# Performance work log

Measured on AMD Instinct MI355X. Metric: run time of the kernel, lower is better.

The kernel has to match this reference:

```python
import jax, jax.numpy as jnp
import numpy as np

B, D, H, R, OUT = 16384, 1024, 4, 1024, 10
LN_EPS = 1e-5


def setup_inputs() -> dict:
    key = jax.random.key(0)
    ks = jax.random.split(key, 20)
    s_in = 1.0 / np.sqrt(D)
    s_hid = 1.0 / np.sqrt(H * R)
    inp = {
        'x': jax.random.normal(ks[0], (B, D), dtype=jnp.float32),
        # block 1
        'wr1': jax.random.normal(ks[1], (H, R, D), dtype=jnp.float32) * s_in,
        'br1': jnp.zeros((H, R), dtype=jnp.float32),
        'wl1': jax.random.normal(ks[2], (H, R, D), dtype=jnp.float32) * s_in,
        'bl1': jnp.zeros((H, R), dtype=jnp.float32),
        'we1': jax.random.normal(ks[3], (D, H * R), dtype=jnp.float32) * s_hid,
        'be1': jnp.zeros((D,), dtype=jnp.float32),
        'g1': jnp.ones((D,), dtype=jnp.float32),
        'b1': jnp.zeros((D,), dtype=jnp.float32),
        # block 2
        'wr2': jax.random.normal(ks[4], (H, R, D), dtype=jnp.float32) * s_in,
        'br2': jnp.zeros((H, R), dtype=jnp.float32),
        'wl2': jax.random.normal(ks[5], (H, R, D), dtype=jnp.float32) * s_in,
        'bl2': jnp.zeros((H, R), dtype=jnp.float32),
        'we2': jax.random.normal(ks[6], (D, H * R), dtype=jnp.float32) * s_hid,
        'be2': jnp.zeros((D,), dtype=jnp.float32),
        'g2': jnp.ones((D,), dtype=jnp.float32),
        'b2': jnp.zeros((D,), dtype=jnp.float32),
        # final linear
        'wf': jax.random.normal(ks[7], (OUT, D), dtype=jnp.float32) * s_in,
        'bf': jnp.zeros((OUT,), dtype=jnp.float32),
    }
    return inp


def _bilinear_block(x, wr, br, wl, bl, we, be):
    # per-basis right/left projections batched into one einsum each: [B,D] x [H,R,D] -> [B,H,R]
    right = jnp.einsum('bd,hrd->bhr', x, wr) + br
    left = jnp.einsum('bd,hrd->bhr', x, wl) + bl
    # elementwise bilinear interaction, concat bases along last dim -> [B, H*R]
    inter = (right * left).reshape(x.shape[0], -1)
    return inter @ we.T + be  # [B, D_out]


def _layernorm(x, g, b):
    mu = jnp.mean(x, axis=-1, keepdims=True)
    var = jnp.mean(jnp.square(x - mu), axis=-1, keepdims=True)
    return (x - mu) * jax.lax.rsqrt(var + LN_EPS) * g + b


def reference(x, wr1, br1, wl1, bl1, we1, be1, g1, b1,
              wr2, br2, wl2, bl2, we2, be2, g2, b2, wf, bf):
    # block 1: bilinear + residual + layernorm
    h = _layernorm(x + _bilinear_block(x, wr1, br1, wl1, bl1, we1, be1), g1, b1)
    # block 2
    h = _layernorm(h + _bilinear_block(h, wr2, br2, wl2, bl2, we2, be2), g2, b2)
    # final linear head
    return h @ wf.T + bf
```

## Files before the change

### kernel.cpp

```cpp
#include <hip/hip_runtime.h>
#include <hip/hip_fp16.h>

#define DEV static __device__ __forceinline__

typedef _Float16 f16;
typedef _Float16 f16x8 __attribute__((ext_vector_type(8)));
typedef _Float16 f16x4 __attribute__((ext_vector_type(4)));
typedef float f32x4 __attribute__((ext_vector_type(4)));

constexpr int BATCH = 16384;
constexpr int D = 1024;
constexpr int HR = 4096;
constexpr int NOUT = 10;

__global__ void k_f32_to_f16(const float* __restrict__ src, f16* __restrict__ dst, int n4) {
    int i = blockIdx.x * blockDim.x + threadIdx.x;
    int stride = gridDim.x * blockDim.x;
    for (; i < n4; i += stride) {
        float4 v = reinterpret_cast<const float4*>(src)[i];
        f16x4 h;
        h[0] = (f16)v.x; h[1] = (f16)v.y; h[2] = (f16)v.z; h[3] = (f16)v.w;
        reinterpret_cast<f16x4*>(dst)[i] = h;
    }
}

DEV void stage16(void* lds, const void* g) {
    __builtin_amdgcn_global_load_lds(
        (const __attribute__((address_space(1))) void*)g,
        (__attribute__((address_space(3))) void*)lds,
        16, 0, 0);
}

DEV const char* src_ptr(const void* base, int tid, int row0, int rowBytes) {
    const int r = tid >> 2;
    const int cb = ((tid & 3) << 4) ^ (((r >> 1) & 3) << 4);
    return (const char*)base + (size_t)(row0 + r) * rowBytes + cb;
}

DEV int xcd_swz(int bid, int nwg) {
    const int cpx = nwg >> 3;
    return (bid & 7) * cpx + (bid >> 3);
}

__global__ __launch_bounds__(512, 2) void k_gemm_dual(
    const f16* __restrict__ Xh, const f16* __restrict__ Wr, const f16* __restrict__ Wl,
    const float* __restrict__ br, const float* __restrict__ bl,
    f16* __restrict__ inter, int MT)
{
    extern __shared__ __align__(16) char smem[];
    constexpr int K = 1024, NT = K / 32;
    constexpr int BUF = 32 * 1024;

    const int swz = xcd_swz(blockIdx.x, gridDim.x);
    const int mt = swz % MT, nt = swz / MT;
    const int m0 = mt * 256, n0 = nt * 128;
    const int tid = threadIdx.x;
    const int wid = tid >> 6, lane = tid & 63;
    const int wm = wid >> 2, wn = wid & 3;
    const int fr = lane & 15, fq = lane >> 4;
    const int colb = (fq << 4) ^ (((fr >> 1) & 3) << 4);

    const char* sA0 = src_ptr(Xh, tid, m0,       2048);
    const char* sA1 = src_ptr(Xh, tid, m0 + 128, 2048);
    const char* sR  = src_ptr(Wr, tid, n0,       2048);
    const char* sL  = src_ptr(Wl, tid, n0,       2048);
    const int dA0 = tid * 16, dA1 = 8192 + tid * 16;
    const int dR = 16384 + tid * 16, dL = 24576 + tid * 16;

    f32x4 accR[8][2] = {};
    f32x4 accL[8][2] = {};

    for (int t = 0; t < 2; ++t) {
        char* b = smem + t * BUF;
        const long ko = (long)t * 64;
        stage16(b + dA0, sA0 + ko);  stage16(b + dA1, sA1 + ko);
        stage16(b + dR,  sR  + ko);  stage16(b + dL,  sL  + ko);
    }
    asm volatile("s_waitcnt vmcnt(4)" ::: "memory");
    __builtin_amdgcn_s_barrier();

    int cur = 0;
    long koff = 128;
    for (int t = 0; t < NT; ++t) {
        char* base = smem + cur * BUF;
        const int stg = cur ? cur - 1 : 2;
        char* nb = smem + stg * BUF;
        const bool pf = (t + 2) < NT;

        f16x8 a[4], bR[2], bL[2];
#pragma unroll
        for (int m = 0; m < 4; ++m)
            a[m] = *(const f16x8*)(base + (wm * 128 + m * 16 + fr) * 64 + colb);
#pragma unroll
        for (int n = 0; n < 2; ++n) {
            bR[n] = *(const f16x8*)(base + 16384 + (wn * 32 + n * 16 + fr) * 64 + colb);
            bL[n] = *(const f16x8*)(base + 24576 + (wn * 32 + n * 16 + fr) * 64 + colb);
        }
        if (pf) { stage16(nb + dA0, sA0 + koff);  stage16(nb + dA1, sA1 + koff); }
        __builtin_amdgcn_s_barrier();
        __builtin_amdgcn_s_setprio(1);
#pragma unroll
        for (int m = 0; m < 4; ++m)
#pragma unroll
            for (int n = 0; n < 2; ++n) {
                accR[m][n] = __builtin_amdgcn_mfma_f32_16x16x32_f16(a[m], bR[n], accR[m][n], 0, 0, 0);
                accL[m][n] = __builtin_amdgcn_mfma_f32_16x16x32_f16(a[m], bL[n], accL[m][n], 0, 0, 0);
            }
        __builtin_amdgcn_s_setprio(0);
        __builtin_amdgcn_s_barrier();

        f16x8 a2[4];
#pragma unroll
        for (int m = 0; m < 4; ++m)
            a2[m] = *(const f16x8*)(base + (wm * 128 + (4 + m) * 16 + fr) * 64 + colb);
        if (pf) { stage16(nb + dR, sR + koff);  stage16(nb + dL, sL + koff); }
        __builtin_amdgcn_s_barrier();
        __builtin_amdgcn_s_setprio(1);
#pragma unroll
        for (int m = 0; m < 4; ++m)
#pragma unroll
            for (int n = 0; n < 2; ++n) {
                accR[4 + m][n] = __builtin_amdgcn_mfma_f32_16x16x32_f16(a2[m], bR[n], accR[4 + m][n], 0, 0, 0);
                accL[4 + m][n] = __builtin_amdgcn_mfma_f32_16x16x32_f16(a2[m], bL[n], accL[4 + m][n], 0, 0, 0);
            }
        __builtin_amdgcn_s_setprio(0);
        if (t < NT - 1) {
            if (pf) asm volatile("s_waitcnt vmcnt(4)" ::: "memory");
            else    asm volatile("s_waitcnt vmcnt(0)" ::: "memory");
        }
        __builtin_amdgcn_s_barrier();

        cur = (cur == 2) ? 0 : cur + 1;
        koff += 64;
    }

#pragma unroll
    for (int n = 0; n < 2; ++n) {
        const int gc = n0 + wn * 32 + n * 16 + fr;
        const float brv = br[gc], blv = bl[gc];
#pragma unroll
        for (int m = 0; m < 8; ++m) {
            const int gr0 = m0 + wm * 128 + m * 16 + fq * 4;
#pragma unroll
            for (int j = 0; j < 4; ++j) {
                const float rv = accR[m][n][j] + brv;
                const float lv = accL[m][n][j] + blv;
                inter[(size_t)(gr0 + j) * HR + gc] = (f16)(rv * lv);
            }
        }
    }
}

__global__ __launch_bounds__(512, 2) void k_gemm_expand(
    const f16* __restrict__ Ain, const f16* __restrict__ Wt,
    const float* __restrict__ be, f16* __restrict__ E, int MT)
{
    extern __shared__ __align__(16) char smem[];
    constexpr int K = HR, NT = K / 32;
    constexpr int BUF = 32 * 1024;

    const int swz = xcd_swz(blockIdx.x, gridDim.x);
    const int mt = swz % MT, nt = swz / MT;
    const int m0 = mt * 256, n0 = nt * 256;
    const int tid = threadIdx.x;
    const int wid = tid >> 6, lane = tid & 63;
    const int wm = wid >> 2, wn = wid & 3;
    const int fr = lane & 15, fq = lane >> 4;
    const int colb = (fq << 4) ^ (((fr >> 1) & 3) << 4);

    const char* sA0 = src_ptr(Ain, tid, m0,       8192);
    const char* sA1 = src_ptr(Ain, tid, m0 + 128, 8192);
    const char* sB0 = src_ptr(Wt,  tid, n0,       8192);
    const char* sB1 = src_ptr(Wt,  tid, n0 + 128, 8192);
    const int dA0 = tid * 16, dA1 = 8192 + tid * 16;
    const int dB0 = 16384 + tid * 16, dB1 = 24576 + tid * 16;

    f32x4 acc[8][4] = {};

    for (int t = 0; t < 2; ++t) {
        char* b = smem + t * BUF;
        const long ko = (long)t * 64;
        stage16(b + dA0, sA0 + ko);  stage16(b + dA1, sA1 + ko);
        stage16(b + dB0, sB0 + ko);  stage16(b + dB1, sB1 + ko);
    }
    asm volatile("s_waitcnt vmcnt(4)" ::: "memory");
    __builtin_amdgcn_s_barrier();

    int cur = 0;
    long koff = 128;
    for (int t = 0; t < NT; ++t) {
        char* base = smem + cur * BUF;
        const int stg = cur ? cur - 1 : 2;
        char* nb = smem + stg * BUF;
        const bool pf = (t + 2) < NT;

        f16x8 a[4], bv[4];
#pragma unroll
        for (int m = 0; m < 4; ++m)
            a[m] = *(const f16x8*)(base + (wm * 128 + m * 16 + fr) * 64 + colb);
#pragma unroll
        for (int n = 0; n < 4; ++n)
            bv[n] = *(const f16x8*)(base + 16384 + (wn * 64 + n * 16 + fr) * 64 + colb);
        if (pf) { stage16(nb + dA0, sA0 + koff);  stage16(nb + dA1, sA1 + koff); }
        __builtin_amdgcn_s_barrier();
        __builtin_amdgcn_s_setprio(1);
#pragma unroll
        for (int m = 0; m < 4; ++m)
#pragma unroll
            for (int n = 0; n < 4; ++n)
                acc[m][n] = __builtin_amdgcn_mfma_f32_16x16x32_f16(a[m], bv[n], acc[m][n], 0, 0, 0);
        __builtin_amdgcn_s_setprio(0);
        __builtin_amdgcn_s_barrier();

        f16x8 a2[4];
#pragma unroll
        for (int m = 0; m < 4; ++m)
            a2[m] = *(const f16x8*)(base + (wm * 128 + (4 + m) * 16 + fr) * 64 + colb);
        if (pf) { stage16(nb + dB0, sB0 + koff);  stage16(nb + dB1, sB1 + koff); }
        __builtin_amdgcn_s_barrier();
        __builtin_amdgcn_s_setprio(1);
#pragma unroll
        for (int m = 0; m < 4; ++m)
#pragma unroll
            for (int n = 0; n < 4; ++n)
                acc[4 + m][n] = __builtin_amdgcn_mfma_f32_16x16x32_f16(a2[m], bv[n], acc[4 + m][n], 0, 0, 0);
        __builtin_amdgcn_s_setprio(0);
        if (t < NT - 1) {
            if (pf) asm volatile("s_waitcnt vmcnt(4)" ::: "memory");
            else    asm volatile("s_waitcnt vmcnt(0)" ::: "memory");
        }
        __builtin_amdgcn_s_barrier();

        cur = (cur == 2) ? 0 : cur + 1;
        koff += 64;
    }

#pragma unroll
    for (int n = 0; n < 4; ++n) {
        const int gc = n0 + wn * 64 + n * 16 + fr;
        const float bev = be[gc];
#pragma unroll
        for (int m = 0; m < 8; ++m) {
            const int gr0 = m0 + wm * 128 + m * 16 + fq * 4;
#pragma unroll
            for (int j = 0; j < 4; ++j)
                E[(size_t)(gr0 + j) * D + gc] = (f16)(acc[m][n][j] + bev);
        }
    }
}

template <typename TR>
__global__ __launch_bounds__(256) void k_ln(
    const TR* __restrict__ X, const f16* __restrict__ Eb,
    const float* __restrict__ g, const float* __restrict__ bb,
    f16* __restrict__ Hh)
{
    const int wid = threadIdx.x >> 6, lane = threadIdx.x & 63;
    const int row = blockIdx.x * 4 + wid;
    const TR* xr = X + (size_t)row * D;
    const f16* er = Eb + (size_t)row * D;
    float v[16];
    float s = 0.f, sq = 0.f;
#pragma unroll
    for (int k = 0; k < 16; ++k) {
        const int c = lane + 64 * k;
        v[k] = (float)xr[c] + (float)er[c];
        s += v[k];
        sq += v[k] * v[k];
    }
#pragma unroll
    for (int off = 32; off; off >>= 1) {
        s += __shfl_down(s, off);
        sq += __shfl_down(sq, off);
    }
    s = __shfl(s, 0);
    sq = __shfl(sq, 0);
    const float mu = s * (1.0f / D);
    const float var = sq * (1.0f / D) - mu * mu;
    const float rs = rsqrtf(var + 1e-5f);
    f16* hh = Hh + (size_t)row * D;
#pragma unroll
    for (int k = 0; k < 16; ++k) {
        const int c = lane + 64 * k;
        const float o = (v[k] - mu) * rs * g[c] + bb[c];
        hh[c] = (f16)o;
    }
}

__global__ __launch_bounds__(256) void k_head(
    const f16* __restrict__ Hf, const float* __restrict__ Wf,
    const float* __restrict__ bf, float* __restrict__ outp)
{
    __shared__ float wfs[NOUT * D];
    for (int i = threadIdx.x; i < NOUT * D; i += 256) wfs[i] = Wf[i];
    __syncthreads();
    const int wid = threadIdx.x >> 6, lane = threadIdx.x & 63;
    const int row = blockIdx.x * 4 + wid;
    const f16* hr = Hf + (size_t)row * D;
    float hv[16];
#pragma unroll
    for (int k = 0; k < 16; ++k) hv[k] = (float)hr[lane + 64 * k];
#pragma unroll
    for (int j = 0; j < NOUT; ++j) {
        float p = 0.f;
#pragma unroll
        for (int k = 0; k < 16; ++k) p += hv[k] * wfs[j * D + lane + 64 * k];
#pragma unroll
        for (int off = 32; off; off >>= 1) p += __shfl_down(p, off);
        if (lane == 0) outp[(size_t)row * NOUT + j] = p + bf[j];
    }
}

extern "C" void kernel_launch(void* const* d_in, const int* in_sizes, int n_in,
                              void* d_out, int out_size, void* d_ws, size_t ws_size,
                              hipStream_t stream) {
    (void)in_sizes; (void)n_in; (void)out_size;
    const float* x   = (const float*)d_in[0];
    const float* wr1 = (const float*)d_in[1];
    const float* br1 = (const float*)d_in[2];
    const float* wl1 = (const float*)d_in[3];
    const float* bl1 = (const float*)d_in[4];
    const float* we1 = (const float*)d_in[5];
    const float* be1 = (const float*)d_in[6];
    const float* g1  = (const float*)d_in[7];
    const float* b1  = (const float*)d_in[8];
    const float* wr2 = (const float*)d_in[9];
    const float* br2 = (const float*)d_in[10];
    const float* wl2 = (const float*)d_in[11];
    const float* bl2 = (const float*)d_in[12];
    const float* we2 = (const float*)d_in[13];
    const float* be2 = (const float*)d_in[14];
    const float* g2  = (const float*)d_in[15];
    const float* b2  = (const float*)d_in[16];
    const float* wf  = (const float*)d_in[17];
    const float* bf  = (const float*)d_in[18];
    float* outp = (float*)d_out;

    constexpr size_t SZ_W16 = (size_t)HR * D * sizeof(f16);
    constexpr size_t SZ_A16 = (size_t)BATCH * D * sizeof(f16);
    constexpr int SMEM = 3 * 32 * 1024;

    hipFuncSetAttribute((const void*)k_gemm_dual,   hipFuncAttributeMaxDynamicSharedMemorySize, SMEM);
    hipFuncSetAttribute((const void*)k_gemm_expand, hipFuncAttributeMaxDynamicSharedMemorySize, SMEM);

    char* p = (char*)d_ws;
    f16* wrh = (f16*)p; p += SZ_W16;
    f16* wlh = (f16*)p; p += SZ_W16;
    f16* weh = (f16*)p; p += SZ_W16;
    f16* xh  = (f16*)p; p += SZ_A16;
    f16* h1h = (f16*)p; p += SZ_A16;
    f16* Eh  = (f16*)p; p += SZ_A16;
    f16* interh = (f16*)p;
    const size_t base = (size_t)(p - (char*)d_ws);
    const size_t avail = ws_size > base ? ws_size - base : 0;

    int CH = 1024;
    if ((size_t)16384 * HR * sizeof(f16) <= avail) CH = 16384;
    else if ((size_t)8192 * HR * sizeof(f16) <= avail) CH = 8192;
    else if ((size_t)4096 * HR * sizeof(f16) <= avail) CH = 4096;
    else if ((size_t)2048 * HR * sizeof(f16) <= avail) CH = 2048;

    f16* h2h = xh;
    const int nch = BATCH / CH;
    const int MT = CH / 256;
    const int gDual = MT * (HR / 128);
    const int gExp  = MT * (D / 256);

    k_f32_to_f16<<<2048, 256, 0, stream>>>(x,   xh,  BATCH * D / 4);
    k_f32_to_f16<<<1024, 256, 0, stream>>>(wr1, wrh, HR * D / 4);
    k_f32_to_f16<<<1024, 256, 0, stream>>>(wl1, wlh, HR * D / 4);
    k_f32_to_f16<<<1024, 256, 0, stream>>>(we1, weh, HR * D / 4);

    for (int c = 0; c < nch; ++c) {
        k_gemm_dual<<<gDual, 512, SMEM, stream>>>(xh + (size_t)c * CH * D, wrh, wlh, br1, bl1, interh, MT);
        k_gemm_expand<<<gExp, 512, SMEM, stream>>>(interh, weh, be1, Eh + (size_t)c * CH * D, MT);
    }
    k_ln<float><<<BATCH / 4, 256, 0, stream>>>(x, Eh, g1, b1, h1h);

    k_f32_to_f16<<<1024, 256, 0, stream>>>(wr2, wrh, HR * D / 4);
    k_f32_to_f16<<<1024, 256, 0, stream>>>(wl2, wlh, HR * D / 4);
    k_f32_to_f16<<<1024, 256, 0, stream>>>(we2, weh, HR * D / 4);

    for (int c = 0; c < nch; ++c) {
        k_gemm_dual<<<gDual, 512, SMEM, stream>>>(h1h + (size_t)c * CH * D, wrh, wlh, br2, bl2, interh, MT);
        k_gemm_expand<<<gExp, 512, SMEM, stream>>>(interh, weh, be2, Eh + (size_t)c * CH * D, MT);
    }
    k_ln<f16><<<BATCH / 4, 256, 0, stream>>>(h1h, Eh, g2, b2, h2h);

    k_head<<<BATCH / 4, 256, 0, stream>>>(h2h, wf, bf, outp);
}
```

Baseline: 969.5 us.

## Switch GEMMs to 32x32x16 MFMA with fragment-ordered LDS staging layout

Both the dual-projection GEMM and the expand GEMM now use the 32x32x16 f16 MFMA instead of 16x16x32. The global-to-LDS staging address mapping is rewritten so each lane's fragment sits contiguously in LDS (lane*16 offsets), which replaces the XOR-swizzled row reads. The larger MFMA cuts instruction count and LDS fragment loads per FLOP. The catch is that the contiguous layout may bring back bank conflicts, and the epilogues must match the new 32x32 accumulator layout.

Result: slower. 1.035 ms (+6.7%).

```diff
diff --git a/kernel.cpp b/kernel.cpp
--- a/kernel.cpp
+++ b/kernel.cpp
@@ -7,6 +7,7 @@
 typedef _Float16 f16x8 __attribute__((ext_vector_type(8)));
 typedef _Float16 f16x4 __attribute__((ext_vector_type(4)));
 typedef float f32x4 __attribute__((ext_vector_type(4)));
+typedef float f32x16 __attribute__((ext_vector_type(16)));
 
 constexpr int BATCH = 16384;
 constexpr int D = 1024;
@@ -31,10 +32,13 @@
         16, 0, 0);
 }
 
-DEV const char* src_ptr(const void* base, int tid, int row0, int rowBytes) {
-    const int r = tid >> 2;
-    const int cb = ((tid & 3) << 4) ^ (((r >> 1) & 3) << 4);
-    return (const char*)base + (size_t)(row0 + r) * rowBytes + cb;
+DEV const char* src_ptr(const void* base, int u, int row0, int rowBytes) {
+    const int msub = u >> 7;
+    const int kstep = (u >> 6) & 1;
+    const int half = (u >> 5) & 1;
+    const int row5 = u & 31;
+    return (const char*)base + (size_t)(row0 + msub * 32 + row5) * rowBytes
+           + kstep * 32 + half * 16;
 }
 
 DEV int xcd_swz(int bid, int nwg) {
@@ -57,8 +61,6 @@
     const int tid = threadIdx.x;
     const int wid = tid >> 6, lane = tid & 63;
     const int wm = wid >> 2, wn = wid & 3;
-    const int fr = lane & 15, fq = lane >> 4;
-    const int colb = (fq << 4) ^ (((fr >> 1) & 3) << 4);
 
     const char* sA0 = src_ptr(Xh, tid, m0,       2048);
     const char* sA1 = src_ptr(Xh, tid, m0 + 128, 2048);
@@ -67,8 +69,11 @@
     const int dA0 = tid * 16, dA1 = 8192 + tid * 16;
     const int dR = 16384 + tid * 16, dL = 24576 + tid * 16;
 
-    f32x4 accR[8][2] = {};
-    f32x4 accL[8][2] = {};
+    const int aoff = wm * 8192 + lane * 16;
+    const int boff = wn * 2048 + lane * 16;
+
+    f32x16 accR[4] = {};
+    f32x16 accL[4] = {};
 
     for (int t = 0; t < 2; ++t) {
         char* b = smem + t * BUF;
@@ -87,42 +92,36 @@
         char* nb = smem + stg * BUF;
         const bool pf = (t + 2) < NT;
 
-        f16x8 a[4], bR[2], bL[2];
-#pragma unroll
-        for (int m = 0; m < 4; ++m)
-            a[m] = *(const f16x8*)(base + (wm * 128 + m * 16 + fr) * 64 + colb);
-#pragma unroll
-        for (int n = 0; n < 2; ++n) {
-            bR[n] = *(const f16x8*)(base + 16384 + (wn * 32 + n * 16 + fr) * 64 + colb);
-            bL[n] = *(const f16x8*)(base + 24576 + (wn * 32 + n * 16 + fr) * 64 + colb);
-        }
+        f16x8 a[4], bR, bL;
+#pragma unroll
+        for (int m = 0; m < 4; ++m)
+            a[m] = *(const f16x8*)(base + aoff + m * 2048);
+        bR = *(const f16x8*)(base + 16384 + boff);
+        bL = *(const f16x8*)(base + 24576 + boff);
         if (pf) { stage16(nb + dA0, sA0 + koff);  stage16(nb + dA1, sA1 + koff); }
         __builtin_amdgcn_s_barrier();
         __builtin_amdgcn_s_setprio(1);
 #pragma unroll
-        for (int m = 0; m < 4; ++m)
-#pragma unroll
-            for (int n = 0; n < 2; ++n) {
-                accR[m][n] = __builtin_amdgcn_mfma_f32_16x16x32_f16(a[m], bR[n], accR[m][n], 0, 0, 0);
-                accL[m][n] = __builtin_amdgcn_mfma_f32_16x16x32_f16(a[m], bL[n], accL[m][n], 0, 0, 0);
-            }
+        for (int m = 0; m < 4; ++m) {
+            accR[m] = __builtin_amdgcn_mfma_f32_32x32x16_f16(a[m], bR, accR[m], 0, 0, 0);
+            accL[m] = __builtin_amdgcn_mfma_f32_32x32x16_f16(a[m], bL, accL[m], 0, 0, 0);
+        }
         __builtin_amdgcn_s_setprio(0);
         __builtin_amdgcn_s_barrier();
 
-        f16x8 a2[4];
-#pragma unroll
-        for (int m = 0; m < 4; ++m)
-            a2[m] = *(const f16x8*)(base + (wm * 128 + (4 + m) * 16 + fr) * 64 + colb);
+#pragma unroll
+        for (int m = 0; m < 4; ++m)
+            a[m] = *(const f16x8*)(base + aoff + m * 2048 + 1024);
+        bR = *(const f16x8*)(base + 16384 + boff + 1024);
+        bL = *(const f16x8*)(base + 24576 + boff + 1024);
         if (pf) { stage16(nb + dR, sR + koff);  stage16(nb + dL, sL + koff); }
         __builtin_amdgcn_s_barrier();
         __builtin_amdgcn_s_setprio(1);
 #pragma unroll
-        for (int m = 0; m < 4; ++m)
-#pragma unroll
-            for (int n = 0; n < 2; ++n) {
-                accR[4 + m][n] = __builtin_amdgcn_mfma_f32_16x16x32_f16(a2[m], bR[n], accR[4 + m][n], 0, 0, 0);
-                accL[4 + m][n] = __builtin_amdgcn_mfma_f32_16x16x32_f16(a2[m], bL[n], accL[4 + m][n], 0, 0, 0);
-            }
+        for (int m = 0; m < 4; ++m) {
+            accR[m] = __builtin_amdgcn_mfma_f32_32x32x16_f16(a[m], bR, accR[m], 0, 0, 0);
+            accL[m] = __builtin_amdgcn_mfma_f32_32x32x16_f16(a[m], bL, accL[m], 0, 0, 0);
+        }
         __builtin_amdgcn_s_setprio(0);
         if (t < NT - 1) {
             if (pf) asm volatile("s_waitcnt vmcnt(4)" ::: "memory");
@@ -134,19 +133,17 @@
         koff += 64;
     }
 
-#pragma unroll
-    for (int n = 0; n < 2; ++n) {
-        const int gc = n0 + wn * 32 + n * 16 + fr;
-        const float brv = br[gc], blv = bl[gc];
-#pragma unroll
-        for (int m = 0; m < 8; ++m) {
-            const int gr0 = m0 + wm * 128 + m * 16 + fq * 4;
-#pragma unroll
-            for (int j = 0; j < 4; ++j) {
-                const float rv = accR[m][n][j] + brv;
-                const float lv = accL[m][n][j] + blv;
-                inter[(size_t)(gr0 + j) * HR + gc] = (f16)(rv * lv);
-            }
+    const int col = n0 + wn * 32 + (lane & 31);
+    const float brv = br[col], blv = bl[col];
+#pragma unroll
+    for (int m = 0; m < 4; ++m) {
+        const int R0 = m0 + wm * 128 + m * 32 + 4 * (lane >> 5);
+#pragma unroll
+        for (int r = 0; r < 16; ++r) {
+            const int row = R0 + (r & 3) + 8 * (r >> 2);
+            const float rv = accR[m][r] + brv;
+            const float lv = accL[m][r] + blv;
+            inter[(size_t)row * HR + col] = (f16)(rv * lv);
         }
     }
 }
@@ -165,8 +162,6 @@
     const int tid = threadIdx.x;
     const int wid = tid >> 6, lane = tid & 63;
     const int wm = wid >> 2, wn = wid & 3;
-    const int fr = lane & 15, fq = lane >> 4;
-    const int colb = (fq << 4) ^ (((fr >> 1) & 3) << 4);
 
     const char* sA0 = src_ptr(Ain, tid, m0,       8192);
     const char* sA1 = src_ptr(Ain, tid, m0 + 128, 8192);
@@ -175,7 +170,10 @@
     const int dA0 = tid * 16, dA1 = 8192 + tid * 16;
     const int dB0 = 16384 + tid * 16, dB1 = 24576 + tid * 16;
 
-    f32x4 acc[8][4] = {};
+    const int aoff = wm * 8192 + lane * 16;
+    const int boff = wn * 4096 + lane * 16;
+
+    f32x16 acc[4][2] = {};
 
     for (int t = 0; t < 2; ++t) {
         char* b = smem + t * BUF;
@@ -194,36 +192,38 @@
         char* nb = smem + stg * BUF;
         const bool pf = (t + 2) < NT;
 
-        f16x8 a[4], bv[4];
-#pragma unroll
-        for (int m = 0; m < 4; ++m)
-            a[m] = *(const f16x8*)(base + (wm * 128 + m * 16 + fr) * 64 + colb);
-#pragma unroll
-        for (int n = 0; n < 4; ++n)
-            bv[n] = *(const f16x8*)(base + 16384 + (wn * 64 + n * 16 + fr) * 64 + colb);
+        f16x8 a[4], bv[2];
+#pragma unroll
+        for (int m = 0; m < 4; ++m)
+            a[m] = *(const f16x8*)(base + aoff + m * 2048);
+#pragma unroll
+        for (int n = 0; n < 2; ++n)
+            bv[n] = *(const f16x8*)(base + 16384 + boff + n * 2048);
         if (pf) { stage16(nb + dA0, sA0 + koff);  stage16(nb + dA1, sA1 + koff); }
         __builtin_amdgcn_s_barrier();
         __builtin_amdgcn_s_setprio(1);
 #pragma unroll
         for (int m = 0; m < 4; ++m)
 #pragma unroll
-            for (int n = 0; n < 4; ++n)
-                acc[m][n] = __builtin_amdgcn_mfma_f32_16x16x32_f16(a[m], bv[n], acc[m][n], 0, 0, 0);
+            for (int n = 0; n < 2; ++n)
+                acc[m][n] = __builtin_amdgcn_mfma_f32_32x32x16_f16(a[m], bv[n], acc[m][n], 0, 0, 0);
         __builtin_amdgcn_s_setprio(0);
         __builtin_amdgcn_s_barrier();
 
-        f16x8 a2[4];
-#pragma unroll
-        for (int m = 0; m < 4; ++m)
-            a2[m] = *(const f16x8*)(base + (wm * 128 + (4 + m) * 16 + fr) * 64 + colb);
+#pragma unroll
+        for (int m = 0; m < 4; ++m)
+            a[m] = *(const f16x8*)(base + aoff + m * 2048 + 1024);
+#pragma unroll
+        for (int n = 0; n < 2; ++n)
+            bv[n] = *(const f16x8*)(base + 16384 + boff + n * 2048 + 1024);
         if (pf) { stage16(nb + dB0, sB0 + koff);  stage16(nb + dB1, sB1 + koff); }
         __builtin_amdgcn_s_barrier();
         __builtin_amdgcn_s_setprio(1);
 #pragma unroll
         for (int m = 0; m < 4; ++m)
 #pragma unroll
-            for (int n = 0; n < 4; ++n)
-                acc[4 + m][n] = __builtin_amdgcn_mfma_f32_16x16x32_f16(a2[m], bv[n], acc[4 + m][n], 0, 0, 0);
+            for (int n = 0; n < 2; ++n)
+                acc[m][n] = __builtin_amdgcn_mfma_f32_32x32x16_f16(a[m], bv[n], acc[m][n], 0, 0, 0);
         __builtin_amdgcn_s_setprio(0);
         if (t < NT - 1) {
             if (pf) asm volatile("s_waitcnt vmcnt(4)" ::: "memory");
@@ -236,15 +236,17 @@
     }
 
 #pragma unroll
-    for (int n = 0; n < 4; ++n) {
-        const int gc = n0 + wn * 64 + n * 16 + fr;
-        const float bev = be[gc];
-#pragma unroll
-        for (int m = 0; m < 8; ++m) {
-            const int gr0 = m0 + wm * 128 + m * 16 + fq * 4;
-#pragma unroll
-            for (int j = 0; j < 4; ++j)
-                E[(size_t)(gr0 + j) * D + gc] = (f16)(acc[m][n][j] + bev);
+    for (int n = 0; n < 2; ++n) {
+        const int col = n0 + wn * 64 + n * 32 + (lane & 31);
+        const float bev = be[col];
+#pragma unroll
+        for (int m = 0; m < 4; ++m) {
+            const int R0 = m0 + wm * 128 + m * 32 + 4 * (lane >> 5);
+#pragma unroll
+            for (int r = 0; r < 16; ++r) {
+                const int row = R0 + (r & 3) + 8 * (r >> 2);
+                E[(size_t)row * D + col] = (f16)(acc[m][n][r] + bev);
+            }
         }
     }
 }
```
